# Kernel optimization log

Hardware: AMD Instinct MI355X
Metric: run time of the kernel (lower is better)

The kernel has to match this reference:

```python
import jax, jax.numpy as jnp
from jax import lax
import numpy as np

B, CIN, COUT, H, W, KH, KW = 32, 256, 256, 56, 56, 3, 3
STRIDE = (1, 1)
PADDING = ((1, 1), (1, 1))
DILATION = (1, 1)


def setup_inputs() -> dict:
    key = jax.random.key(0)
    k1, k2, k3, k4 = jax.random.split(key, 4)
    x = jax.random.normal(k1, (B, CIN, H, W), dtype=jnp.float32)
    # int8 symmetric-quantized weights, stored as int32 values in [-127, 127]
    weight_q = jax.random.randint(k2, (COUT, CIN, KH, KW), -127, 128, dtype=jnp.int32)
    weight_scale = jax.random.uniform(k3, (), dtype=jnp.float32, minval=0.001, maxval=0.02)
    fan_in = CIN * KH * KW
    bound = 1.0 / np.sqrt(fan_in)
    bias = jax.random.uniform(k4, (COUT,), dtype=jnp.float32, minval=-bound, maxval=bound)
    return {"x": x, "weight_q": weight_q, "weight_scale": weight_scale, "bias": bias}


def reference(x, weight_q, weight_scale, bias):
    # Per-tensor symmetric int8 quantization of the activation.
    x_scale = jnp.max(jnp.abs(x)) / 127.0
    x_q = jnp.clip(jnp.round(x / x_scale), -127.0, 127.0)  # int8 values in fp32
    # max |acc| <= 127*127*256*9 < 2^24 per partial, use fp32 conv as reference).
    acc = lax.conv_general_dilated(
        x_q,
        weight_q.astype(jnp.float32),
        window_strides=STRIDE,
        padding=PADDING,
        rhs_dilation=DILATION,
        dimension_numbers=("NCHW", "OIHW", "NCHW"),
    )
    # Dequantize and add bias.
    y = acc * (x_scale * weight_scale) + bias[None, :, None, None]
    return y
```

## Files before the change

kernel.cpp:

```cpp
#include <hip/hip_runtime.h>
#include <stdint.h>

#define CIN   256
#define COUT  256
#define HH    56
#define WW    56
#define BB    32
#define HP    58
#define WP    58
#define KTOT  2304
#define NPIX  (BB*HH*WW)
#define OHW   (HH*WW)

#define WS_AMAX_OFF   0
#define WS_WPACK_OFF  256
#define WPACK_BYTES   (COUT*KTOT)
#define WS_XPAD_OFF   (1<<20)
#define XPAD_BYTES    (BB*HP*WP*CIN)

typedef __attribute__((ext_vector_type(4))) int i32x4;

__global__ void absmax_kernel(const float* __restrict__ x,
                              unsigned int* __restrict__ amax, int n4) {
  int tid = blockIdx.x * blockDim.x + threadIdx.x;
  int stride = gridDim.x * blockDim.x;
  const float4* x4 = (const float4*)x;
  float m = 0.0f;
  for (int i = tid; i < n4; i += stride) {
    float4 v = x4[i];
    m = fmaxf(m, fmaxf(fmaxf(fabsf(v.x), fabsf(v.y)),
                       fmaxf(fabsf(v.z), fabsf(v.w))));
  }
#pragma unroll
  for (int off = 32; off >= 1; off >>= 1)
    m = fmaxf(m, __shfl_xor(m, off, 64));
  __shared__ float red[4];
  int lane = threadIdx.x & 63, wv = threadIdx.x >> 6;
  if (lane == 0) red[wv] = m;
  __syncthreads();
  if (threadIdx.x == 0) {
    float mm = fmaxf(fmaxf(red[0], red[1]), fmaxf(red[2], red[3]));
    atomicMax(amax, __float_as_uint(mm));
  }
}

__global__ void quant_kernel(const float* __restrict__ x,
                             const unsigned int* __restrict__ amax,
                             int8_t* __restrict__ xpad) {
  const int cb = blockIdx.x;
  const int h  = blockIdx.y;
  const int b  = blockIdx.z;
  const int ci0 = cb * 64;
  const float xs = __uint_as_float(*amax) / 127.0f;
  __shared__ __align__(16) int8_t t[56 * 68];
  const int tid = threadIdx.x;
  for (int e = tid; e < 64 * 56; e += 256) {
    int ci = e / 56;
    int w  = e - ci * 56;
    float v = x[(((b * CIN) + ci0 + ci) * HH + h) * WW + w];
    float q = rintf(v / xs);
    q = fminf(127.0f, fmaxf(-127.0f, q));
    t[w * 68 + ci] = (int8_t)(int)q;
  }
  __syncthreads();
  uint8_t* dst = (uint8_t*)xpad;
  for (int e = tid; e < 56 * 16; e += 256) {
    int w = e >> 4, c4 = e & 15;
    unsigned int v = *(const unsigned int*)&t[w * 68 + c4 * 4];
    *(unsigned int*)(dst + ((((b * HP) + h + 1) * WP + (w + 1)) << 8) + ci0 + c4 * 4) = v;
  }
}

__global__ void wpack_kernel(const int* __restrict__ wq, int8_t* __restrict__ wp) {
  int i = blockIdx.x * 256 + threadIdx.x;
  int ci   = i & 255;
  int t    = i >> 8;
  int khkw = t % 9;
  int co   = t / 9;
  wp[i] = (int8_t)wq[(co * CIN + ci) * 9 + khkw];
}

__global__ __launch_bounds__(256, 2)
void conv_kernel(const int8_t* __restrict__ xpad, const int8_t* __restrict__ wp,
                 const unsigned int* __restrict__ amax,
                 const float* __restrict__ wscale,
                 const float* __restrict__ bias, float* __restrict__ out) {
  __shared__ __align__(16) int8_t As[2][128 * 64];
  __shared__ __align__(16) int8_t Bs[2][128 * 64];

  const int tid  = threadIdx.x;
  const int lane = tid & 63;
  const int wv   = tid >> 6;
  const int wm   = wv >> 1;
  const int wn   = wv & 1;

  int bx = blockIdx.x;
  const int cpx = gridDim.x >> 3;
  bx = (bx & 7) * cpx + (bx >> 3);
  const int m0 = (bx & 1) << 7;
  const int n0 = (bx >> 1) << 7;

  const int8_t* gA[2];
  const int8_t* gB[2];
#pragma unroll
  for (int i = 0; i < 2; ++i) {
    int s = i * 256 + tid;
    int r = s >> 2;
    int slog = (s & 3) ^ ((r >> 1) & 3);
    gA[i] = wp + (m0 + r) * KTOT + slog * 16;
    int p  = n0 + r;
    int ow = p % 56;
    int t1 = p / 56;
    int oh = t1 % 56;
    int b  = t1 / 56;
    gB[i] = xpad + (((b * HP + oh) * WP) + ow) * 256 + slog * 16;
  }

  const int rr = lane & 15;
  const int physseg = ((lane >> 4) ^ ((rr >> 1) & 3)) << 4;

  auto stage = [&](int bsel, int kk) {
    int khkw = kk >> 2;
    int kh = khkw / 3;
    int kw = khkw - kh * 3;
    int koffB = ((kh * WP + kw) << 8) + ((kk & 3) << 6);
    int koffA = kk << 6;
#pragma unroll
    for (int i = 0; i < 2; ++i) {
      __builtin_amdgcn_global_load_lds(
          (const __attribute__((address_space(1))) void*)(gA[i] + koffA),
          (__attribute__((address_space(3))) void*)&As[bsel][i * 4096 + wv * 1024],
          16, 0, 0);
      __builtin_amdgcn_global_load_lds(
          (const __attribute__((address_space(1))) void*)(gB[i] + koffB),
          (__attribute__((address_space(3))) void*)&Bs[bsel][i * 4096 + wv * 1024],
          16, 0, 0);
    }
  };

  i32x4 acc[4][4] = {};

  stage(0, 0);
  __syncthreads();
  int buf = 0;
  for (int kk = 0; kk < 36; ++kk) {
    if (kk < 35) stage(buf ^ 1, kk + 1);
    const int8_t* Ab = As[buf];
    const int8_t* Bb = Bs[buf];
    i32x4 a[4], b[4];
#pragma unroll
    for (int mi = 0; mi < 4; ++mi)
      a[mi] = *(const i32x4*)(Ab + (((wm << 6) + (mi << 4) + rr) << 6) + physseg);
#pragma unroll
    for (int ni = 0; ni < 4; ++ni)
      b[ni] = *(const i32x4*)(Bb + (((wn << 6) + (ni << 4) + rr) << 6) + physseg);
#pragma unroll
    for (int mi = 0; mi < 4; ++mi)
#pragma unroll
      for (int ni = 0; ni < 4; ++ni)
        acc[mi][ni] = __builtin_amdgcn_mfma_i32_16x16x64_i8(a[mi], b[ni], acc[mi][ni], 0, 0, 0);
    __syncthreads();
    buf ^= 1;
  }

  const float xs = __uint_as_float(*amax) / 127.0f;
  const float cmul = xs * wscale[0];
#pragma unroll
  for (int ni = 0; ni < 4; ++ni) {
    int p  = n0 + (wn << 6) + (ni << 4) + rr;
    int ow = p % 56;
    int t1 = p / 56;
    int oh = t1 % 56;
    int b  = t1 / 56;
    int obase = b * (COUT * OHW) + oh * 56 + ow;
#pragma unroll
    for (int mi = 0; mi < 4; ++mi) {
      int co = m0 + (wm << 6) + (mi << 4) + ((lane >> 4) << 2);
#pragma unroll
      for (int j = 0; j < 4; ++j) {
        out[obase + (co + j) * OHW] = (float)acc[mi][ni][j] * cmul + bias[co + j];
      }
    }
  }
}

extern "C" void kernel_launch(void* const* d_in, const int* in_sizes, int n_in,
                              void* d_out, int out_size, void* d_ws, size_t ws_size,
                              hipStream_t stream) {
  const float* x       = (const float*)d_in[0];
  const int*   wq      = (const int*)d_in[1];
  const float* wscale  = (const float*)d_in[2];
  const float* bias    = (const float*)d_in[3];
  float* out = (float*)d_out;

  uint8_t* ws = (uint8_t*)d_ws;
  unsigned int* amax = (unsigned int*)(ws + WS_AMAX_OFF);
  int8_t* wp   = (int8_t*)(ws + WS_WPACK_OFF);
  int8_t* xpad = (int8_t*)(ws + WS_XPAD_OFF);

  hipMemsetAsync(amax, 0, 4, stream);
  hipMemsetAsync(xpad, 0, XPAD_BYTES, stream);

  absmax_kernel<<<2048, 256, 0, stream>>>(x, amax, (NPIX * CIN) / 4);
  quant_kernel<<<dim3(4, 56, 32), 256, 0, stream>>>(x, amax, xpad);
  wpack_kernel<<<WPACK_BYTES / 256, 256, 0, stream>>>(wq, wp);
  conv_kernel<<<(NPIX / 128) * (COUT / 128), 256, 0, stream>>>(xpad, wp, amax, wscale, bias, out);
}
```

Baseline: 319.5 us.

## Triple-buffer conv LDS pipeline, zero only halo, drop atomics and memsets

The conv main loop moves from double to triple buffering of the LDS tiles. It uses explicit vmcnt waits and a single barrier per iteration, so global loads run two stages ahead of the MFMA work, and occupancy is set to 3 blocks per CU. The full memset of the padded int8 activation buffer is replaced by a small kernel that zeroes only the halo border. The absmax reduction now writes per-block partials that the weight-pack kernel folds, which removes the atomic and the amax memset. The trade-off is more LDS per block (48KB) and hand-written wait counts that must match the number of loads in flight.

Measured after the change: 320.1 us. No clear change (+0.2%).

```diff
diff --git a/kernel.cpp b/kernel.cpp
--- a/kernel.cpp
+++ b/kernel.cpp
@@ -13,7 +13,8 @@
 #define OHW   (HH*WW)
 
 #define WS_AMAX_OFF   0
-#define WS_WPACK_OFF  256
+#define WS_PART_OFF   256
+#define WS_WPACK_OFF  16384
 #define WPACK_BYTES   (COUT*KTOT)
 #define WS_XPAD_OFF   (1<<20)
 #define XPAD_BYTES    (BB*HP*WP*CIN)
@@ -21,7 +22,7 @@
 typedef __attribute__((ext_vector_type(4))) int i32x4;
 
 __global__ void absmax_kernel(const float* __restrict__ x,
-                              unsigned int* __restrict__ amax, int n4) {
+                              float* __restrict__ partial, int n4) {
   int tid = blockIdx.x * blockDim.x + threadIdx.x;
   int stride = gridDim.x * blockDim.x;
   const float4* x4 = (const float4*)x;
@@ -38,10 +39,52 @@
   int lane = threadIdx.x & 63, wv = threadIdx.x >> 6;
   if (lane == 0) red[wv] = m;
   __syncthreads();
-  if (threadIdx.x == 0) {
-    float mm = fmaxf(fmaxf(red[0], red[1]), fmaxf(red[2], red[3]));
-    atomicMax(amax, __float_as_uint(mm));
-  }
+  if (threadIdx.x == 0)
+    partial[blockIdx.x] = fmaxf(fmaxf(red[0], red[1]), fmaxf(red[2], red[3]));
+}
+
+__global__ void wpack_kernel(const int* __restrict__ wq, int8_t* __restrict__ wp,
+                             const float* __restrict__ partial,
+                             unsigned int* __restrict__ amax) {
+  if (blockIdx.x == 0) {
+    float m = 0.0f;
+    for (int i = threadIdx.x; i < 2048; i += 256) m = fmaxf(m, partial[i]);
+#pragma unroll
+    for (int off = 32; off >= 1; off >>= 1)
+      m = fmaxf(m, __shfl_xor(m, off, 64));
+    __shared__ float red[4];
+    int lane = threadIdx.x & 63, wvv = threadIdx.x >> 6;
+    if (lane == 0) red[wvv] = m;
+    __syncthreads();
+    if (threadIdx.x == 0)
+      *amax = __float_as_uint(fmaxf(fmaxf(red[0], red[1]), fmaxf(red[2], red[3])));
+  }
+  int i = blockIdx.x * 256 + threadIdx.x;
+  int ci   = i & 255;
+  int t    = i >> 8;
+  int khkw = t % 9;
+  int co   = t / 9;
+  wp[i] = (int8_t)wq[(co * CIN + ci) * 9 + khkw];
+}
+
+__global__ void halo_kernel(int8_t* __restrict__ xpad) {
+  int idx = blockIdx.x * 256 + threadIdx.x;
+  int b = idx / 3648;
+  int r = idx - b * 3648;
+  long byteoff;
+  if (r < 1856) {
+    int row = (r < 928) ? 0 : 57;
+    int c   = (r < 928) ? r : r - 928;
+    byteoff = ((long)(b * HP + row) * WP) * 256 + (long)c * 16;
+  } else {
+    int rc = r - 1856;
+    int h  = (rc >> 5) + 1;
+    int t  = rc & 31;
+    int w  = (t < 16) ? 0 : 57;
+    int c16 = t & 15;
+    byteoff = ((long)((b * HP + h) * WP + w)) * 256 + (long)c16 * 16;
+  }
+  *(int4*)(xpad + byteoff) = int4{0, 0, 0, 0};
 }
 
 __global__ void quant_kernel(const float* __restrict__ x,
@@ -71,22 +114,13 @@
   }
 }
 
-__global__ void wpack_kernel(const int* __restrict__ wq, int8_t* __restrict__ wp) {
-  int i = blockIdx.x * 256 + threadIdx.x;
-  int ci   = i & 255;
-  int t    = i >> 8;
-  int khkw = t % 9;
-  int co   = t / 9;
-  wp[i] = (int8_t)wq[(co * CIN + ci) * 9 + khkw];
-}
-
-__global__ __launch_bounds__(256, 2)
+__global__ __launch_bounds__(256, 3)
 void conv_kernel(const int8_t* __restrict__ xpad, const int8_t* __restrict__ wp,
                  const unsigned int* __restrict__ amax,
                  const float* __restrict__ wscale,
                  const float* __restrict__ bias, float* __restrict__ out) {
-  __shared__ __align__(16) int8_t As[2][128 * 64];
-  __shared__ __align__(16) int8_t Bs[2][128 * 64];
+  __shared__ __align__(16) int8_t As[3][128 * 64];
+  __shared__ __align__(16) int8_t Bs[3][128 * 64];
 
   const int tid  = threadIdx.x;
   const int lane = tid & 63;
@@ -141,12 +175,17 @@
   i32x4 acc[4][4] = {};
 
   stage(0, 0);
-  __syncthreads();
-  int buf = 0;
-  for (int kk = 0; kk < 36; ++kk) {
-    if (kk < 35) stage(buf ^ 1, kk + 1);
-    const int8_t* Ab = As[buf];
-    const int8_t* Bb = Bs[buf];
+  stage(1, 1);
+  asm volatile("s_waitcnt vmcnt(4)" ::: "memory");
+  __builtin_amdgcn_s_barrier();
+  __builtin_amdgcn_sched_barrier(0);
+
+  int cur = 0, stg = 2;
+  for (int kt = 0; kt < 36; ++kt) {
+    if (kt < 34) stage(stg, kt + 2);
+
+    const int8_t* Ab = As[cur];
+    const int8_t* Bb = Bs[cur];
     i32x4 a[4], b[4];
 #pragma unroll
     for (int mi = 0; mi < 4; ++mi)
@@ -159,8 +198,15 @@
 #pragma unroll
       for (int ni = 0; ni < 4; ++ni)
         acc[mi][ni] = __builtin_amdgcn_mfma_i32_16x16x64_i8(a[mi], b[ni], acc[mi][ni], 0, 0, 0);
-    __syncthreads();
-    buf ^= 1;
+
+    if (kt < 34)       asm volatile("s_waitcnt vmcnt(4)" ::: "memory");
+    else if (kt == 34) asm volatile("s_waitcnt vmcnt(0)" ::: "memory");
+    if (kt < 35) {
+      __builtin_amdgcn_s_barrier();
+      __builtin_amdgcn_sched_barrier(0);
+    }
+    cur = (cur == 2) ? 0 : cur + 1;
+    stg = (stg == 2) ? 0 : stg + 1;
   }
 
   const float xs = __uint_as_float(*amax) / 127.0f;
@@ -195,14 +241,13 @@
 
   uint8_t* ws = (uint8_t*)d_ws;
   unsigned int* amax = (unsigned int*)(ws + WS_AMAX_OFF);
+  float* partial     = (float*)(ws + WS_PART_OFF);
   int8_t* wp   = (int8_t*)(ws + WS_WPACK_OFF);
   int8_t* xpad = (int8_t*)(ws + WS_XPAD_OFF);
 
-  hipMemsetAsync(amax, 0, 4, stream);
-  hipMemsetAsync(xpad, 0, XPAD_BYTES, stream);
-
-  absmax_kernel<<<2048, 256, 0, stream>>>(x, amax, (NPIX * CIN) / 4);
+  absmax_kernel<<<2048, 256, 0, stream>>>(x, partial, (NPIX * CIN) / 4);
+  wpack_kernel<<<WPACK_BYTES / 256, 256, 0, stream>>>(wq, wp, partial, amax);
+  halo_kernel<<<456, 256, 0, stream>>>(xpad);
   quant_kernel<<<dim3(4, 56, 32), 256, 0, stream>>>(x, amax, xpad);
-  wpack_kernel<<<WPACK_BYTES / 256, 256, 0, stream>>>(wq, wp);
   conv_kernel<<<(NPIX / 128) * (COUT / 128), 256, 0, stream>>>(xpad, wp, amax, wscale, bias, out);
 }
```
